# Kernel tuning notes

Measured on AMD Instinct MI355X. Metric: run time of the kernel, lower is better.

## Reference

```python
import jax, jax.numpy as jnp
import numpy as np
from jax import lax

B, T = 256, 256
FD = (768, 74, 35)      # text, audio, vision input feature dims
HD = (128, 64, 64)      # LSTM hidden sizes
LEN = sum(HD)           # 256, fused feature dim
TW = 2                  # time_window
EXT = TW * LEN + 1      # 513, extended_dim
RANK = 24
OUT = 1


def setup_inputs() -> dict:
    key = jax.random.key(0)
    ks = iter(jax.random.split(key, 32))
    def n(shape, scale=0.05):
        return jax.random.normal(next(ks), shape, dtype=jnp.float32) * scale
    inp = {
        "text": n((B, T, FD[0]), 1.0),
        "audio": n((B, T, FD[1]), 1.0),
        "vision": n((B, T, FD[2]), 1.0),
    }
    # LSTM params per subnet: W_ih [4H, D], W_hh [4H, H], combined bias [4H]
    for tag, d, h in (("t", FD[0], HD[0]), ("a", FD[1], HD[1]), ("v", FD[2], HD[2])):
        inp[f"Wih_{tag}"] = n((4 * h, d))
        inp[f"Whh_{tag}"] = n((4 * h, h))
        inp[f"b_{tag}"] = n((4 * h,))
    inp["W1"] = n((RANK * OUT, LEN))
    inp["b1"] = n((RANK * OUT,))
    inp["W2"] = n((RANK * OUT, EXT))
    inp["b2"] = n((RANK * OUT,))
    inp["fw"] = n((1, RANK), 1.0)  # fusion_weights, xavier_normal-like
    return inp


def _lstm_seq(x, Wih, Whh, b):
    # x: [B, T, D] -> all hidden states [B, T, H]; torch gate order i,f,g,o
    Bn = x.shape[0]
    H = Whh.shape[1]
    h0 = jnp.zeros((Bn, H), x.dtype)
    def step(carry, xt):
        h, c = carry
        g = xt @ Wih.T + h @ Whh.T + b
        i, f, gg, o = jnp.split(g, 4, axis=-1)
        c = jax.nn.sigmoid(f) * c + jax.nn.sigmoid(i) * jnp.tanh(gg)
        h = jax.nn.sigmoid(o) * jnp.tanh(c)
        return (h, c), h
    _, hs = lax.scan(step, (h0, h0), jnp.swapaxes(x, 0, 1))
    return jnp.swapaxes(hs, 0, 1)


def reference(text, audio, vision,
              Wih_t, Whh_t, b_t, Wih_a, Whh_a, b_a, Wih_v, Whh_v, b_v,
              W1, b1, W2, b2, fw):
    # SubNets (dropout is identity in eval mode)
    audio_h = _lstm_seq(audio, Wih_a, Whh_a, b_a)
    video_h = _lstm_seq(vision, Wih_v, Whh_v, b_v)
    text_h = _lstm_seq(text, Wih_t, Whh_t, b_t)
    z = jnp.concatenate((audio_h, video_h, text_h), axis=2)  # [B, T, LEN]
    # time_extend with time_window=2: [ones, z[:, i], z[:, (i+1) % T]]
    ones = jnp.ones((z.shape[0], z.shape[1], 1), z.dtype)
    shifts = [jnp.roll(z, -j, axis=1) for j in range(TW)]
    z_ext = jnp.concatenate([ones] + shifts, axis=2)  # [B, T, EXT]
    # fusion loop over idx (stride=1 -> all T), vectorized as batched GEMM + mean
    a = jnp.einsum('btl,rl->btr', z, W1) + b1          # [B, T, RANK*OUT]
    bb = jnp.einsum('bte,re->btr', z_ext, W2) + b2     # [B, T, RANK*OUT]
    z_fusion = (a * bb).mean(axis=1)                   # sum_i/len(idx)
    z_fusion = z_fusion.reshape(-1, RANK, OUT)
    z_output = jnp.einsum('r,bro->bo', fw[0], z_fusion)
    output = z_output.reshape(-1, OUT)
    norm = jnp.sum(jnp.linalg.norm(z.reshape(z.shape[0], -1), axis=1)) / z.shape[0]
    return output, norm
```

## Files before the change

### kernel.cpp

```cpp
#include <hip/hip_runtime.h>
#include <math.h>


typedef unsigned short ushortT;
typedef short bf16x8 __attribute__((ext_vector_type(8)));
typedef float f32x4 __attribute__((ext_vector_type(4)));

__device__ __forceinline__ unsigned int f2bf(float f) {
  unsigned int u = __float_as_uint(f);
  u += 0x7FFFu + ((u >> 16) & 1u);
  return u >> 16;
}
__device__ __forceinline__ unsigned int pk2bf(float lo, float hi) {
  return f2bf(lo) | (f2bf(hi) << 16);
}
__device__ __forceinline__ float bf2f(ushortT u) {
  return __uint_as_float(((unsigned int)u) << 16);
}

template <int KP, int KIN, int HR>
__device__ __forceinline__ void cvt_range(const float* __restrict__ src,
                                          ushortT* __restrict__ dst,
                                          int i, int total) {
  if (i >= total) return;
  if constexpr (HR == 0 && KP == KIN) {
    dst[i] = (ushortT)f2bf(src[i]);
  } else {
    const int row = i / KP, c = i - row * KP;
    const int srow = HR ? ((row & 3) * HR + (row >> 2)) : row;
    const float v = (c < KIN) ? src[(size_t)srow * KIN + c] : 0.f;
    dst[i] = (ushortT)f2bf(v);
  }
}

__global__ __launch_bounds__(256) void prep_k(
    const float* __restrict__ Wih_t, const float* __restrict__ Whh_t,
    const float* __restrict__ Wih_a, const float* __restrict__ Whh_a,
    const float* __restrict__ Wih_v, const float* __restrict__ Whh_v,
    const float* __restrict__ audio, const float* __restrict__ vision,
    ushortT* __restrict__ Wt768, ushortT* __restrict__ WhhT16,
    ushortT* __restrict__ WA16, ushortT* __restrict__ WhhA16,
    ushortT* __restrict__ WV16, ushortT* __restrict__ WhhV16,
    ushortT* __restrict__ A16a, ushortT* __restrict__ A16v) {
  const int b = blockIdx.x, tid = threadIdx.x;
  if (b < 1536)       cvt_range<768, 768, 128>(Wih_t, Wt768, b * 256 + tid, 393216);
  else if (b < 1792)  cvt_range<128, 128, 0>(Whh_t, WhhT16, (b - 1536) * 256 + tid, 65536);
  else if (b < 1856)  cvt_range<64, 64, 0>(Whh_a, WhhA16, (b - 1792) * 256 + tid, 16384);
  else if (b < 1920)  cvt_range<64, 64, 0>(Whh_v, WhhV16, (b - 1856) * 256 + tid, 16384);
  else if (b < 2016)  cvt_range<96, 74, 64>(Wih_a, WA16, (b - 1920) * 256 + tid, 24576);
  else if (b < 2080)  cvt_range<64, 35, 64>(Wih_v, WV16, (b - 2016) * 256 + tid, 16384);
  else if (b < 26656) cvt_range<96, 74, 0>(audio, A16a, (b - 2080) * 256 + tid, 6291456);
  else                cvt_range<64, 35, 0>(vision, A16v, (b - 26656) * 256 + tid, 4194304);
}

#define SA2 40
__global__ __launch_bounds__(512) void gemm_text2_k(const float* __restrict__ X,
                                                    const ushortT* __restrict__ W16,
                                                    const float* __restrict__ bias,
                                                    ushortT* __restrict__ Y16) {
  const int K = 768, N = 512;
  __shared__ __align__(16) ushortT As[128 * SA2];
  __shared__ __align__(16) ushortT Bs[256 * SA2];
  const unsigned int lin = blockIdx.x;
  const int gb = (int)(lin >> 4), rb = (int)(lin & 15);
  const int m0 = (gb * 8 + (rb & 7)) * 128;
  const int n0 = (rb >> 3) * 256;
  const int tid = threadIdx.x;
  const int wave = tid >> 6, lane = tid & 63;
  const int wr = wave >> 2, wc = wave & 3;
  const int lm = lane & 15, lq = lane >> 4;
  const int arow = tid >> 2, aq = (tid & 3) * 8;
  const int brow = tid >> 1, bq = (tid & 1) * 16;

  const float*   Xp = X + (size_t)(m0 + arow) * K + aq;
  const ushortT* Wp = W16 + (size_t)(n0 + brow) * K + bq;
  uint4* As_w = (uint4*)&As[arow * SA2 + aq];
  uint4* Bs_w = (uint4*)&Bs[brow * SA2 + bq];

  f32x4 acc[4][4];
#pragma unroll
  for (int i = 0; i < 4; i++)
#pragma unroll
    for (int j = 0; j < 4; j++) acc[i][j] = (f32x4){0.f, 0.f, 0.f, 0.f};

  for (int k0 = 0; k0 < K; k0 += 32) {
    const float4 a0 = *(const float4*)(Xp + k0);
    const float4 a1 = *(const float4*)(Xp + k0 + 4);
    const uint4 b0v = *(const uint4*)(Wp + k0);
    const uint4 b1v = *(const uint4*)(Wp + k0 + 8);
    __syncthreads();
    uint4 ao;
    ao.x = pk2bf(a0.x, a0.y); ao.y = pk2bf(a0.z, a0.w);
    ao.z = pk2bf(a1.x, a1.y); ao.w = pk2bf(a1.z, a1.w);
    As_w[0] = ao;
    Bs_w[0] = b0v;
    Bs_w[1] = b1v;
    __syncthreads();
    bf16x8 af[4], bfv[4];
#pragma unroll
    for (int mt = 0; mt < 4; mt++)
      af[mt] = *(const bf16x8*)&As[(wr * 64 + mt * 16 + lm) * SA2 + lq * 8];
#pragma unroll
    for (int nt = 0; nt < 4; nt++)
      bfv[nt] = *(const bf16x8*)&Bs[(wc * 64 + nt * 16 + lm) * SA2 + lq * 8];
#pragma unroll
    for (int mt = 0; mt < 4; mt++)
#pragma unroll
      for (int nt = 0; nt < 4; nt++)
        acc[mt][nt] = __builtin_amdgcn_mfma_f32_16x16x32_bf16(af[mt], bfv[nt], acc[mt][nt], 0, 0, 0);
  }
  float biasv[4];
#pragma unroll
  for (int nt = 0; nt < 4; nt++) {
    const int C = n0 + wc * 64 + nt * 16 + lm;
    biasv[nt] = bias[((C & 3) << 7) + (C >> 2)];
  }
#pragma unroll
  for (int mt = 0; mt < 4; mt++) {
#pragma unroll
    for (int nt = 0; nt < 4; nt++) {
      const int row0 = m0 + wr * 64 + mt * 16 + lq * 4;
      const int col = n0 + wc * 64 + nt * 16 + lm;
#pragma unroll
      for (int r = 0; r < 4; r++)
        Y16[(size_t)(row0 + r) * N + col] = (ushortT)f2bf(acc[mt][nt][r] + biasv[nt]);
    }
  }
}

template <int KP, int LOG2H>
__global__ __launch_bounds__(256) void gemm_xp_k(const ushortT* __restrict__ A16,
                                                 const ushortT* __restrict__ B16,
                                                 const float* __restrict__ bias,
                                                 ushortT* __restrict__ Y16) {
  constexpr int SB = KP + 8;
  __shared__ __align__(16) ushortT As[128 * SB];
  __shared__ __align__(16) ushortT Bs[128 * SB];
  const int n0 = blockIdx.x * 128;
  const int m0 = blockIdx.y * 128;
  const int tid = threadIdx.x;
  const int srow = tid >> 1, shalf = tid & 1;
  const int wave = tid >> 6, lane = tid & 63;
  const int wr = wave >> 1, wc = wave & 1;
  const int lm = lane & 15, lq = lane >> 4;

  const uint4* ap = (const uint4*)(A16 + (size_t)(m0 + srow) * KP + shalf * (KP / 2));
  const uint4* bp = (const uint4*)(B16 + (size_t)(n0 + srow) * KP + shalf * (KP / 2));
  uint4* aw = (uint4*)&As[srow * SB + shalf * (KP / 2)];
  uint4* bw = (uint4*)&Bs[srow * SB + shalf * (KP / 2)];
#pragma unroll
  for (int i = 0; i < KP / 16; i++) { aw[i] = ap[i]; bw[i] = bp[i]; }
  __syncthreads();

  constexpr int KC = KP / 32;
  f32x4 acc[4][4];
#pragma unroll
  for (int i = 0; i < 4; i++)
#pragma unroll
    for (int j = 0; j < 4; j++) acc[i][j] = (f32x4){0.f, 0.f, 0.f, 0.f};
#pragma unroll
  for (int ks = 0; ks < KC; ks++) {
    bf16x8 af[4], bfv[4];
#pragma unroll
    for (int mt = 0; mt < 4; mt++)
      af[mt] = *(const bf16x8*)&As[(wr * 64 + mt * 16 + lm) * SB + ks * 32 + lq * 8];
#pragma unroll
    for (int nt = 0; nt < 4; nt++)
      bfv[nt] = *(const bf16x8*)&Bs[(wc * 64 + nt * 16 + lm) * SB + ks * 32 + lq * 8];
#pragma unroll
    for (int mt = 0; mt < 4; mt++)
#pragma unroll
      for (int nt = 0; nt < 4; nt++)
        acc[mt][nt] = __builtin_amdgcn_mfma_f32_16x16x32_bf16(af[mt], bfv[nt], acc[mt][nt], 0, 0, 0);
  }
  float biasv[4];
#pragma unroll
  for (int nt = 0; nt < 4; nt++) {
    const int C = n0 + wc * 64 + nt * 16 + lm;
    biasv[nt] = bias[((C & 3) << LOG2H) + (C >> 2)];
  }
#pragma unroll
  for (int mt = 0; mt < 4; mt++) {
#pragma unroll
    for (int nt = 0; nt < 4; nt++) {
      const int row0 = m0 + wr * 64 + mt * 16 + lq * 4;
      const int col = n0 + wc * 64 + nt * 16 + lm;
#pragma unroll
      for (int r = 0; r < 4; r++)
        Y16[(size_t)(row0 + r) * 256 + col] = (ushortT)f2bf(acc[mt][nt][r] + biasv[nt]);
    }
  }
}

__device__ __forceinline__ void bar_lgkm() {
  asm volatile("s_waitcnt lgkmcnt(0)" ::: "memory");
  __builtin_amdgcn_sched_barrier(0);
  __builtin_amdgcn_s_barrier();
  __builtin_amdgcn_sched_barrier(0);
}

template <int H, int COFF, int CW>
__device__ __forceinline__ void recur_impl5(const ushortT* __restrict__ xp,
                                            const ushortT* __restrict__ Whh,
                                            ushortT* __restrict__ z,
                                            int bblk, char* smem_) {
  constexpr int KC = H / 32;
  constexpr int C4H = 4 * H;
  constexpr int HP = H + 8;
  constexpr int RING = 6;
  constexpr int CRB = H / 8;
  constexpr int FPT = (64 * CRB) / 512;
  constexpr int RS = 256 * C4H;
  ushortT* hbuf = (ushortT*)smem_;
  const int tid = threadIdx.x;
  const int s = tid >> 6, lane = tid & 63;
  const int lm = lane & 15, lq = lane >> 4;
  const int b0 = bblk * 16;
  const bool comp = (s < CW);
  const ushortT* xb = xp + (size_t)(b0 + lq * 4) * RS + (s * 16 + lm) * 4;

  bf16x8 bw[4][KC];
  if (comp) {
#pragma unroll
    for (int g = 0; g < 4; g++)
#pragma unroll
      for (int kc = 0; kc < KC; kc++) {
        const int n = g * H + s * 16 + lm;
        bw[g][kc] = *(const bf16x8*)(Whh + (size_t)n * H + kc * 32 + lq * 8);
      }
  }
  for (int i = tid; i < 16 * HP; i += 512) hbuf[(RING - 1) * 16 * HP + i] = 0;

  uint2 gA[4], gB[4];
  if (comp) {
#pragma unroll
    for (int r = 0; r < 4; r++) {
      gA[r] = *(const uint2*)(xb + (size_t)r * RS);
      gB[r] = *(const uint2*)(xb + (size_t)r * RS + C4H);
    }
  }
  float cst[4] = {0.f, 0.f, 0.f, 0.f};
  __syncthreads();

  auto step = [&](int t, uint2 (&gCur)[4]) {
    if (t >= 4 && (t & 3) == 0) {
      const int t0 = t - 4;
#pragma unroll
      for (int i = 0; i < FPT; i++) {
        const int q = i * 512 + tid;
        const int m = q / (4 * CRB), j = (q / CRB) & 3, cr = q % CRB;
        const uint4 v = *(const uint4*)&hbuf[((t0 + j) % RING) * 16 * HP + m * HP + cr * 8];
        *(uint4*)&z[((size_t)(b0 + m) * 256 + t0 + j) * 256 + COFF + cr * 8] = v;
      }
    }
    if (comp) {
      float ad[4][4];
#pragma unroll
      for (int r = 0; r < 4; r++) {
        const unsigned int w0 = gCur[r].x, w1 = gCur[r].y;
        ad[0][r] = __uint_as_float(w0 << 16);
        ad[1][r] = __uint_as_float(w0 & 0xffff0000u);
        ad[2][r] = __uint_as_float(w1 << 16);
        ad[3][r] = __uint_as_float(w1 & 0xffff0000u);
      }
      const int tn = (t + 2 < 256) ? t + 2 : 255;
#pragma unroll
      for (int r = 0; r < 4; r++)
        gCur[r] = *(const uint2*)(xb + (size_t)r * RS + (size_t)tn * C4H);
      const ushortT* hb = &hbuf[((t + RING - 1) % RING) * 16 * HP + lm * HP];
      bf16x8 af[KC];
#pragma unroll
      for (int kc = 0; kc < KC; kc++) af[kc] = *(const bf16x8*)(hb + kc * 32 + lq * 8);
      f32x4 acc[4];
#pragma unroll
      for (int g = 0; g < 4; g++) acc[g] = (f32x4){0.f, 0.f, 0.f, 0.f};
#pragma unroll
      for (int kc = 0; kc < KC; kc++)
#pragma unroll
        for (int g = 0; g < 4; g++)
          acc[g] = __builtin_amdgcn_mfma_f32_16x16x32_bf16(af[kc], bw[g][kc], acc[g], 0, 0, 0);
      ushortT* hw = &hbuf[(t % RING) * 16 * HP];
      const int col = s * 16 + lm;
#pragma unroll
      for (int r = 0; r < 4; r++) {
        const float iv = acc[0][r] + ad[0][r];
        const float fv = acc[1][r] + ad[1][r];
        const float gg = acc[2][r] + ad[2][r];
        const float ov = acc[3][r] + ad[3][r];
        const float ei = __expf(-iv), ef = __expf(-fv), eg = __expf(-2.f * gg);
        const float pi = 1.f + ei, pf = 1.f + ef, pg = 1.f + eg;
        const float cc = (cst[r] * pi * pg + (1.f - eg) * pf) *
                         __builtin_amdgcn_rcpf(pf * pi * pg);
        cst[r] = cc;
        const float ec = __expf(-2.f * cc), eo = __expf(-ov);
        const float hv = (1.f - ec) * __builtin_amdgcn_rcpf((1.f + eo) * (1.f + ec));
        hw[(lq * 4 + r) * HP + col] = (ushortT)f2bf(hv);
      }
    }
    bar_lgkm();
  };

  for (int t = 0; t < 256; t += 2) {
    step(t, gA);
    step(t + 1, gB);
  }
  {
    const int t0 = 252;
#pragma unroll
    for (int i = 0; i < FPT; i++) {
      const int q = i * 512 + tid;
      const int m = q / (4 * CRB), j = (q / CRB) & 3, cr = q % CRB;
      const uint4 v = *(const uint4*)&hbuf[((t0 + j) % RING) * 16 * HP + m * HP + cr * 8];
      *(uint4*)&z[((size_t)(b0 + m) * 256 + t0 + j) * 256 + COFF + cr * 8] = v;
    }
  }
}

__global__ __launch_bounds__(512, 1) void recur5_k(const ushortT* __restrict__ xpt,
                                                   const ushortT* __restrict__ xpa,
                                                   const ushortT* __restrict__ xpv_,
                                                   const ushortT* __restrict__ Wt,
                                                   const ushortT* __restrict__ Wa,
                                                   const ushortT* __restrict__ Wv,
                                                   ushortT* __restrict__ z) {
  extern __shared__ char smem[];
  const int bid = blockIdx.x;
  if (bid < 16) recur_impl5<128, 128, 8>(xpt, Wt, z, bid, smem);
  else if (bid < 32) recur_impl5<64, 0, 4>(xpa, Wa, z, bid - 16, smem);
  else recur_impl5<64, 64, 4>(xpv_, Wv, z, bid - 32, smem);
}

__global__ __launch_bounds__(192) void fusion_k(const ushortT* __restrict__ z,
                                                const float* __restrict__ W1,
                                                const float* __restrict__ b1,
                                                const float* __restrict__ W2,
                                                const float* __restrict__ b2,
                                                const float* __restrict__ fw,
                                                float* __restrict__ s_acc,
                                                float* __restrict__ sumsq) {
  __shared__ __align__(16) float zs[256 * 36];
  __shared__ float red[8];
  const int tid = threadIdx.x;
  const int b = blockIdx.x >> 3;
  const int t0 = (blockIdx.x & 7) * 32;
  const ushortT* zb = z + (size_t)b * 65536;
  float sq = 0.0f;
  for (int idx = tid; idx < 33 * 256; idx += 192) {
    const int row = idx >> 8, k = idx & 255;
    int t = t0 + row; if (t >= 256) t -= 256;
    const float v = bf2f(zb[t * 256 + k]);
    zs[k * 36 + row] = v;
    if (row < 32) sq += v * v;
  }
  __syncthreads();
  const int dg = tid >> 3;
  const int rg = tid & 7;
  const float* w1p = W1 + dg * 256;
  const float* w2p = W2 + dg * 513;
  float aa[4] = {}, ab1[4] = {}, ab2[4] = {};
#pragma unroll 4
  for (int k = 0; k < 256; k++) {
    const float w1v = w1p[k];
    const float w21 = w2p[1 + k];
    const float w22 = w2p[257 + k];
    const float* zr = &zs[k * 36 + (rg << 2)];
    const float4 za = *(const float4*)zr;
    const float z4 = zr[4];
    aa[0]  += za.x * w1v; aa[1]  += za.y * w1v; aa[2]  += za.z * w1v; aa[3]  += za.w * w1v;
    ab1[0] += za.x * w21; ab1[1] += za.y * w21; ab1[2] += za.z * w21; ab1[3] += za.w * w21;
    ab2[0] += za.y * w22; ab2[1] += za.z * w22; ab2[2] += za.w * w22; ab2[3] += z4   * w22;
  }
  const float b1v = b1[dg];
  const float b2v = b2[dg] + w2p[0];
  const float fwv = fw[dg];
  float s = 0.0f;
#pragma unroll
  for (int i = 0; i < 4; i++) {
    const float a  = aa[i] + b1v;
    const float bb = ab1[i] + ab2[i] + b2v;
    s += a * bb;
  }
  s *= fwv;
#pragma unroll
  for (int off = 32; off > 0; off >>= 1) {
    s  += __shfl_down(s, off);
    sq += __shfl_down(sq, off);
  }
  const int wid = tid >> 6;
  if ((tid & 63) == 0) { red[wid * 2] = s; red[wid * 2 + 1] = sq; }
  __syncthreads();
  if (tid == 0) {
    atomicAdd(&s_acc[b], red[0] + red[2] + red[4]);
    atomicAdd(&sumsq[b], red[1] + red[3] + red[5]);
  }
}

__global__ __launch_bounds__(256) void final_k(const float* __restrict__ s_acc,
                                               const float* __restrict__ sumsq,
                                               float* __restrict__ out) {
  __shared__ float red[4];
  const int tid = threadIdx.x;
  out[tid] = s_acc[tid] * (1.0f / 256.0f);
  float sq = sqrtf(sumsq[tid]);
#pragma unroll
  for (int off = 32; off > 0; off >>= 1) sq += __shfl_down(sq, off);
  if ((tid & 63) == 0) red[tid >> 6] = sq;
  __syncthreads();
  if (tid == 0) out[256] = (red[0] + red[1] + red[2] + red[3]) * (1.0f / 256.0f);
}

extern "C" void kernel_launch(void* const* d_in, const int* in_sizes, int n_in,
                              void* d_out, int out_size, void* d_ws, size_t ws_size,
                              hipStream_t stream) {
  const float* text   = (const float*)d_in[0];
  const float* audio  = (const float*)d_in[1];
  const float* vision = (const float*)d_in[2];
  const float* Wih_t  = (const float*)d_in[3];
  const float* Whh_t  = (const float*)d_in[4];
  const float* b_t    = (const float*)d_in[5];
  const float* Wih_a  = (const float*)d_in[6];
  const float* Whh_a  = (const float*)d_in[7];
  const float* b_a    = (const float*)d_in[8];
  const float* Wih_v  = (const float*)d_in[9];
  const float* Whh_v  = (const float*)d_in[10];
  const float* b_v    = (const float*)d_in[11];
  const float* W1     = (const float*)d_in[12];
  const float* b1     = (const float*)d_in[13];
  const float* W2     = (const float*)d_in[14];
  const float* b2     = (const float*)d_in[15];
  const float* fw     = (const float*)d_in[16];

  ushortT* xpt = (ushortT*)d_ws;
  ushortT* xpa = xpt + (size_t)33554432;
  ushortT* xpv = xpa + (size_t)16777216;
  ushortT* z16 = xpv + (size_t)16777216;
  float* s_acc = (float*)(z16 + (size_t)16777216);
  float* sumsq = s_acc + 256;
  ushortT* WhhT16 = (ushortT*)(sumsq + 256);
  ushortT* WhhA16 = WhhT16 + 65536;
  ushortT* WhhV16 = WhhA16 + 16384;
  ushortT* A16a  = z16;
  ushortT* A16v  = A16a + (size_t)6291456;
  ushortT* Wt768 = A16v + (size_t)4194304;
  ushortT* WA16  = Wt768 + 393216;
  ushortT* WV16  = WA16 + 24576;

  hipMemsetAsync(s_acc, 0, 512 * sizeof(float), stream);

  prep_k<<<43040, 256, 0, stream>>>(Wih_t, Whh_t, Wih_a, Whh_a, Wih_v, Whh_v,
                                    audio, vision,
                                    Wt768, WhhT16, WA16, WhhA16, WV16, WhhV16,
                                    A16a, A16v);

  gemm_text2_k<<<1024, 512, 0, stream>>>(text, Wt768, b_t, xpt);
  gemm_xp_k<96, 6><<<dim3(2, 512), 256, 0, stream>>>(A16a, WA16, b_a, xpa);
  gemm_xp_k<64, 6><<<dim3(2, 512), 256, 0, stream>>>(A16v, WV16, b_v, xpv);
  recur5_k<<<48, 512, 26112, stream>>>(xpt, xpa, xpv, WhhT16, WhhA16, WhhV16, z16);
  fusion_k<<<2048, 192, 0, stream>>>(z16, W1, b1, W2, b2, fw, s_acc, sumsq);
  final_k<<<1, 256, 0, stream>>>(s_acc, sumsq, (float*)d_out);
}
```

Before: 765.1 us.

## Prefetch text GEMM loads, merge audio/vision GEMMs, vectorize fusion weight loads

The text input-projection GEMM now issues the next K-slice's global loads before the LDS compute, overlapping memory latency with MFMA work. The audio and vision projection GEMMs are merged into one launch via a z-dimension split. W2 is split in the prep kernel into aligned 256-wide halves so the fusion kernel can use float4 weight loads instead of scalar ones. These cut launch overhead and load latency, at the cost of extra registers for the prefetch and a larger shared-memory footprint for the merged vision blocks.

```diff
diff --git a/kernel.cpp b/kernel.cpp
--- a/kernel.cpp
+++ b/kernel.cpp
@@ -38,10 +38,12 @@
     const float* __restrict__ Wih_a, const float* __restrict__ Whh_a,
     const float* __restrict__ Wih_v, const float* __restrict__ Whh_v,
     const float* __restrict__ audio, const float* __restrict__ vision,
+    const float* __restrict__ W2,
     ushortT* __restrict__ Wt768, ushortT* __restrict__ WhhT16,
     ushortT* __restrict__ WA16, ushortT* __restrict__ WhhA16,
     ushortT* __restrict__ WV16, ushortT* __restrict__ WhhV16,
-    ushortT* __restrict__ A16a, ushortT* __restrict__ A16v) {
+    ushortT* __restrict__ A16a, ushortT* __restrict__ A16v,
+    float* __restrict__ w2a, float* __restrict__ w2b, float* __restrict__ w2c) {
   const int b = blockIdx.x, tid = threadIdx.x;
   if (b < 1536)       cvt_range<768, 768, 128>(Wih_t, Wt768, b * 256 + tid, 393216);
   else if (b < 1792)  cvt_range<128, 128, 0>(Whh_t, WhhT16, (b - 1536) * 256 + tid, 65536);
@@ -50,7 +52,17 @@
   else if (b < 2016)  cvt_range<96, 74, 64>(Wih_a, WA16, (b - 1920) * 256 + tid, 24576);
   else if (b < 2080)  cvt_range<64, 35, 64>(Wih_v, WV16, (b - 2016) * 256 + tid, 16384);
   else if (b < 26656) cvt_range<96, 74, 0>(audio, A16a, (b - 2080) * 256 + tid, 6291456);
-  else                cvt_range<64, 35, 0>(vision, A16v, (b - 26656) * 256 + tid, 4194304);
+  else if (b < 43040) cvt_range<64, 35, 0>(vision, A16v, (b - 26656) * 256 + tid, 4194304);
+  else {
+    const int i = (b - 43040) * 256 + tid;
+    if (i < 12312) {
+      const int dg = i / 513, c = i - dg * 513;
+      const float v = W2[i];
+      if (c == 0) w2c[dg] = v;
+      else if (c <= 256) w2a[dg * 256 + c - 1] = v;
+      else w2b[dg * 256 + c - 257] = v;
+    }
+  }
 }
 
 #define SA2 40
@@ -83,11 +95,12 @@
 #pragma unroll
     for (int j = 0; j < 4; j++) acc[i][j] = (f32x4){0.f, 0.f, 0.f, 0.f};
 
+  float4 a0 = *(const float4*)(Xp);
+  float4 a1 = *(const float4*)(Xp + 4);
+  uint4 b0v = *(const uint4*)(Wp);
+  uint4 b1v = *(const uint4*)(Wp + 8);
+
   for (int k0 = 0; k0 < K; k0 += 32) {
-    const float4 a0 = *(const float4*)(Xp + k0);
-    const float4 a1 = *(const float4*)(Xp + k0 + 4);
-    const uint4 b0v = *(const uint4*)(Wp + k0);
-    const uint4 b1v = *(const uint4*)(Wp + k0 + 8);
     __syncthreads();
     uint4 ao;
     ao.x = pk2bf(a0.x, a0.y); ao.y = pk2bf(a0.z, a0.w);
@@ -95,6 +108,12 @@
     As_w[0] = ao;
     Bs_w[0] = b0v;
     Bs_w[1] = b1v;
+    if (k0 + 32 < K) {
+      a0 = *(const float4*)(Xp + k0 + 32);
+      a1 = *(const float4*)(Xp + k0 + 36);
+      b0v = *(const uint4*)(Wp + k0 + 32);
+      b1v = *(const uint4*)(Wp + k0 + 40);
+    }
     __syncthreads();
     bf16x8 af[4], bfv[4];
 #pragma unroll
@@ -129,13 +148,12 @@
 }
 
 template <int KP, int LOG2H>
-__global__ __launch_bounds__(256) void gemm_xp_k(const ushortT* __restrict__ A16,
-                                                 const ushortT* __restrict__ B16,
-                                                 const float* __restrict__ bias,
-                                                 ushortT* __restrict__ Y16) {
+__device__ __forceinline__ void gemm_xp_impl(const ushortT* __restrict__ A16,
+                                             const ushortT* __restrict__ B16,
+                                             const float* __restrict__ bias,
+                                             ushortT* __restrict__ Y16,
+                                             ushortT* As, ushortT* Bs) {
   constexpr int SB = KP + 8;
-  __shared__ __align__(16) ushortT As[128 * SB];
-  __shared__ __align__(16) ushortT Bs[128 * SB];
   const int n0 = blockIdx.x * 128;
   const int m0 = blockIdx.y * 128;
   const int tid = threadIdx.x;
@@ -190,6 +208,20 @@
         Y16[(size_t)(row0 + r) * 256 + col] = (ushortT)f2bf(acc[mt][nt][r] + biasv[nt]);
     }
   }
+}
+
+__global__ __launch_bounds__(256) void gemm_av_k(const ushortT* __restrict__ A16a,
+                                                 const ushortT* __restrict__ WA16,
+                                                 const float* __restrict__ b_a,
+                                                 ushortT* __restrict__ xpa,
+                                                 const ushortT* __restrict__ A16v,
+                                                 const ushortT* __restrict__ WV16,
+                                                 const float* __restrict__ b_v,
+                                                 ushortT* __restrict__ xpv) {
+  __shared__ __align__(16) ushortT As[128 * 104];
+  __shared__ __align__(16) ushortT Bs[128 * 104];
+  if (blockIdx.z == 0) gemm_xp_impl<96, 6>(A16a, WA16, b_a, xpa, As, Bs);
+  else gemm_xp_impl<64, 6>(A16v, WV16, b_v, xpv, As, Bs);
 }
 
 __device__ __forceinline__ void bar_lgkm() {
@@ -333,7 +365,9 @@
 __global__ __launch_bounds__(192) void fusion_k(const ushortT* __restrict__ z,
                                                 const float* __restrict__ W1,
                                                 const float* __restrict__ b1,
-                                                const float* __restrict__ W2,
+                                                const float* __restrict__ w2a,
+                                                const float* __restrict__ w2b,
+                                                const float* __restrict__ w2c,
                                                 const float* __restrict__ b2,
                                                 const float* __restrict__ fw,
                                                 float* __restrict__ s_acc,
@@ -356,22 +390,33 @@
   const int dg = tid >> 3;
   const int rg = tid & 7;
   const float* w1p = W1 + dg * 256;
-  const float* w2p = W2 + dg * 513;
+  const float* w2ap = w2a + dg * 256;
+  const float* w2bp = w2b + dg * 256;
   float aa[4] = {}, ab1[4] = {}, ab2[4] = {};
-#pragma unroll 4
-  for (int k = 0; k < 256; k++) {
-    const float w1v = w1p[k];
-    const float w21 = w2p[1 + k];
-    const float w22 = w2p[257 + k];
-    const float* zr = &zs[k * 36 + (rg << 2)];
-    const float4 za = *(const float4*)zr;
-    const float z4 = zr[4];
-    aa[0]  += za.x * w1v; aa[1]  += za.y * w1v; aa[2]  += za.z * w1v; aa[3]  += za.w * w1v;
-    ab1[0] += za.x * w21; ab1[1] += za.y * w21; ab1[2] += za.z * w21; ab1[3] += za.w * w21;
-    ab2[0] += za.y * w22; ab2[1] += za.z * w22; ab2[2] += za.w * w22; ab2[3] += z4   * w22;
+  for (int k = 0; k < 256; k += 4) {
+    const float4 w1v4  = *(const float4*)(w1p + k);
+    const float4 w21v4 = *(const float4*)(w2ap + k);
+    const float4 w22v4 = *(const float4*)(w2bp + k);
+#define FUS_STEP(J, W1C, W21C, W22C)                                   \
+    {                                                                  \
+      const float* zr = &zs[(k + J) * 36 + (rg << 2)];                 \
+      const float4 za = *(const float4*)zr;                            \
+      const float z4 = zr[4];                                          \
+      aa[0] += za.x * (W1C); aa[1] += za.y * (W1C);                    \
+      aa[2] += za.z * (W1C); aa[3] += za.w * (W1C);                    \
+      ab1[0] += za.x * (W21C); ab1[1] += za.y * (W21C);                \
+      ab1[2] += za.z * (W21C); ab1[3] += za.w * (W21C);                \
+      ab2[0] += za.y * (W22C); ab2[1] += za.z * (W22C);                \
+      ab2[2] += za.w * (W22C); ab2[3] += z4 * (W22C);                  \
+    }
+    FUS_STEP(0, w1v4.x, w21v4.x, w22v4.x)
+    FUS_STEP(1, w1v4.y, w21v4.y, w22v4.y)
+    FUS_STEP(2, w1v4.z, w21v4.z, w22v4.z)
+    FUS_STEP(3, w1v4.w, w21v4.w, w22v4.w)
+#undef FUS_STEP
   }
   const float b1v = b1[dg];
-  const float b2v = b2[dg] + w2p[0];
+  const float b2v = b2[dg] + w2c[dg];
   const float fwv = fw[dg];
   float s = 0.0f;
 #pragma unroll
@@ -439,6 +484,9 @@
   ushortT* WhhT16 = (ushortT*)(sumsq + 256);
   ushortT* WhhA16 = WhhT16 + 65536;
   ushortT* WhhV16 = WhhA16 + 16384;
+  float* w2a = (float*)(WhhV16 + 16384);
+  float* w2b = w2a + 6144;
+  float* w2c = w2b + 6144;
   ushortT* A16a  = z16;
   ushortT* A16v  = A16a + (size_t)6291456;
   ushortT* Wt768 = A16v + (size_t)4194304;
@@ -447,15 +495,15 @@
 
   hipMemsetAsync(s_acc, 0, 512 * sizeof(float), stream);
 
-  prep_k<<<43040, 256, 0, stream>>>(Wih_t, Whh_t, Wih_a, Whh_a, Wih_v, Whh_v,
-                                    audio, vision,
+  prep_k<<<43089, 256, 0, stream>>>(Wih_t, Whh_t, Wih_a, Whh_a, Wih_v, Whh_v,
+                                    audio, vision, W2,
                                     Wt768, WhhT16, WA16, WhhA16, WV16, WhhV16,
-                                    A16a, A16v);
+                                    A16a, A16v, w2a, w2b, w2c);
 
   gemm_text2_k<<<1024, 512, 0, stream>>>(text, Wt768, b_t, xpt);
-  gemm_xp_k<96, 6><<<dim3(2, 512), 256, 0, stream>>>(A16a, WA16, b_a, xpa);
-  gemm_xp_k<64, 6><<<dim3(2, 512), 256, 0, stream>>>(A16v, WV16, b_v, xpv);
+  gemm_av_k<<<dim3(2, 512, 2), 256, 0, stream>>>(A16a, WA16, b_a, xpa,
+                                                 A16v, WV16, b_v, xpv);
   recur5_k<<<48, 512, 26112, stream>>>(xpt, xpa, xpv, WhhT16, WhhA16, WhhV16, z16);
-  fusion_k<<<2048, 192, 0, stream>>>(z16, W1, b1, W2, b2, fw, s_acc, sumsq);
+  fusion_k<<<2048, 192, 0, stream>>>(z16, W1, b1, w2a, w2b, w2c, b2, fw, s_acc, sumsq);
   final_k<<<1, 256, 0, stream>>>(s_acc, sumsq, (float*)d_out);
 }
```

After: 750.5 us. Within noise of the previous version (-1.9%).
